# Performance work log

Measured on AMD Instinct MI355X. Metric: run time of the kernel, lower is better.

## Reference

```python
import jax, jax.numpy as jnp
import numpy as np

N = 2_097_152   # number of samples
C = 16          # n_classes
DECAY = 0.8


def setup_inputs() -> dict:
    key = jax.random.key(0)
    k1, k2 = jax.random.split(key)
    logits = jax.random.normal(k1, (N, C), dtype=jnp.float32)
    targets = jax.random.randint(k2, (N,), 0, C)
    weight = jnp.ones((C,), dtype=jnp.float32)  # EMA class-weight buffer
    return {"logits": logits, "targets": targets, "weight": weight}


def reference(logits, targets, weight):
    # Single-pass histogram (replaces the per-class Python loop in the source)
    counts = jax.ops.segment_sum(
        jnp.ones_like(targets, dtype=logits.dtype), targets, num_segments=C
    )  # [C]
    new_w = counts.sum() / counts          # total / per-class count
    new_w = new_w / new_w.sum()            # normalize to sum 1
    w = DECAY * weight + (1.0 - DECAY) * new_w  # EMA-updated weight [C]

    # Weighted cross-entropy, mean reduction (torch semantics:
    # sum(w[y_i] * nll_i) / sum(w[y_i]))
    logp = jax.nn.log_softmax(logits, axis=-1)                       # [N, C]
    nll = -jnp.take_along_axis(logp, targets[:, None], axis=-1)[:, 0]  # [N]
    sw = w[targets]                                                  # [N]
    return jnp.sum(sw * nll) / jnp.sum(sw)
```

## Files before the change

### kernel.cpp

```cpp
#include <hip/hip_runtime.h>

#define NCLS 16
#define DECAY 0.8f

__device__ __forceinline__ float sel16(float4 q0, float4 q1, float4 q2,
                                       float4 q3, int t) {
    float4 sv = (t & 8) ? ((t & 4) ? q3 : q2) : ((t & 4) ? q1 : q0);
    const float lo = (t & 1) ? sv.y : sv.x;
    const float hi = (t & 1) ? sv.w : sv.z;
    return (t & 2) ? hi : lo;
}

__device__ __forceinline__ float esum4(float4 v) {
    return __expf(v.x) + __expf(v.y) + __expf(v.z) + __expf(v.w);
}

__global__ void __launch_bounds__(256, 4)
dwce_fused_kernel(const float4* __restrict__ logits4,
                  const int4*   __restrict__ targets4,
                  float2* __restrict__ partials, int n) {
    __shared__ unsigned int cnt[4][NCLS];
    __shared__ float       snll[4][NCLS];

    const int tid = threadIdx.x;
    const int wid = tid >> 6;
    if (tid < 64) { cnt[tid >> 4][tid & 15] = 0u; snll[tid >> 4][tid & 15] = 0.f; }
    __syncthreads();

    const int gid  = blockIdx.x * blockDim.x + tid;
    const int nth  = gridDim.x * blockDim.x;
    const int ngrp = n >> 2;

    for (int g = gid; g < ngrp; g += nth) {
        const int4 t = targets4[g];
        const float4* base = logits4 + ((size_t)g << 4);
        float4 a0 = base[0],  a1 = base[1],  a2 = base[2],  a3 = base[3];
        float4 b0 = base[4],  b1 = base[5],  b2 = base[6],  b3 = base[7];
        float4 c0 = base[8],  c1 = base[9],  c2 = base[10], c3 = base[11];
        float4 d0 = base[12], d1 = base[13], d2 = base[14], d3 = base[15];

        const float S0 = esum4(a0) + esum4(a1) + esum4(a2) + esum4(a3);
        const float S1 = esum4(b0) + esum4(b1) + esum4(b2) + esum4(b3);
        const float S2 = esum4(c0) + esum4(c1) + esum4(c2) + esum4(c3);
        const float S3 = esum4(d0) + esum4(d1) + esum4(d2) + esum4(d3);

        const float x0 = sel16(a0, a1, a2, a3, t.x);
        const float x1 = sel16(b0, b1, b2, b3, t.y);
        const float x2 = sel16(c0, c1, c2, c3, t.z);
        const float x3 = sel16(d0, d1, d2, d3, t.w);

        atomicAdd(&snll[wid][t.x], __logf(S0) - x0);
        atomicAdd(&snll[wid][t.y], __logf(S1) - x1);
        atomicAdd(&snll[wid][t.z], __logf(S2) - x2);
        atomicAdd(&snll[wid][t.w], __logf(S3) - x3);
        atomicAdd(&cnt[wid][t.x], 1u);
        atomicAdd(&cnt[wid][t.y], 1u);
        atomicAdd(&cnt[wid][t.z], 1u);
        atomicAdd(&cnt[wid][t.w], 1u);
    }
    __syncthreads();

    if (tid < NCLS) {
        const unsigned int c =
            cnt[0][tid] + cnt[1][tid] + cnt[2][tid] + cnt[3][tid];
        const float s =
            snll[0][tid] + snll[1][tid] + snll[2][tid] + snll[3][tid];
        partials[tid * gridDim.x + blockIdx.x] = make_float2((float)c, s);
    }
}

__global__ void __launch_bounds__(1024)
dwce_final_kernel(const float2* __restrict__ partials,
                  const float*  __restrict__ weight,
                  int nb, int n, float* __restrict__ out) {
    const int tid  = threadIdx.x;
    const int c    = tid >> 6;
    const int lane = tid & 63;

    float  cacc = 0.f;
    double sacc = 0.0;
    for (int b = lane; b < nb; b += 64) {
        const float2 p = partials[c * nb + b];
        cacc += p.x;
        sacc += (double)p.y;
    }
    #pragma unroll
    for (int off = 32; off > 0; off >>= 1) {
        cacc += __shfl_xor(cacc, off);
        sacc += __shfl_xor(sacc, off);
    }

    __shared__ float  scnt[NCLS];
    __shared__ double ssum[NCLS];
    if (lane == 0) { scnt[c] = cacc; ssum[c] = sacc; }
    __syncthreads();

    if (tid < NCLS) {
        const float  cn = scnt[tid];
        const double sn = ssum[tid];

        const float raw = (float)n / cn;
        float s = raw;
        s += __shfl_xor(s, 1);
        s += __shfl_xor(s, 2);
        s += __shfl_xor(s, 4);
        s += __shfl_xor(s, 8);
        const float w = DECAY * weight[tid] + (1.0f - DECAY) * (raw / s);

        double A = (double)w * sn;
        double B = (double)w * (double)cn;
        A += __shfl_xor(A, 1); B += __shfl_xor(B, 1);
        A += __shfl_xor(A, 2); B += __shfl_xor(B, 2);
        A += __shfl_xor(A, 4); B += __shfl_xor(B, 4);
        A += __shfl_xor(A, 8); B += __shfl_xor(B, 8);
        if (tid == 0) out[0] = (float)(A / B);
    }
}

extern "C" void kernel_launch(void* const* d_in, const int* in_sizes, int n_in,
                              void* d_out, int out_size, void* d_ws, size_t ws_size,
                              hipStream_t stream) {
    const float* logits  = (const float*)d_in[0];
    const int*   targets = (const int*)d_in[1];
    const float* weight  = (const float*)d_in[2];
    float* out = (float*)d_out;

    float2* partials = (float2*)d_ws;

    const int n = in_sizes[1];

    int nb = 2048;
    const int ws_cap = (int)(ws_size / (NCLS * sizeof(float2)));
    if (nb > ws_cap) nb = ws_cap;
    if (nb < 1) nb = 1;

    dwce_fused_kernel<<<nb, 256, 0, stream>>>((const float4*)logits,
                                              (const int4*)targets,
                                              partials, n);
    dwce_final_kernel<<<1, 1024, 0, stream>>>(partials, weight, nb, n, out);
}
```

Before: 38.65 us.

## Process two rows per thread from split halves with more blocks

Each thread now handles two rows, one from each half of the batch, instead of four consecutive rows. Adjacent threads therefore read adjacent 64-byte rows, which improves coalescing over the earlier 256-byte stride, and per-thread register pressure drops. The launch-bounds occupancy hint goes from 4 to 8 and the grid doubles to 4096 blocks. The trade-offs are scalar target loads instead of int4, a larger partials buffer for the final reduction, and an odd n leaving its last row unprocessed.

```diff
diff --git a/kernel.cpp b/kernel.cpp
--- a/kernel.cpp
+++ b/kernel.cpp
@@ -15,9 +15,9 @@
     return __expf(v.x) + __expf(v.y) + __expf(v.z) + __expf(v.w);
 }
 
-__global__ void __launch_bounds__(256, 4)
+__global__ void __launch_bounds__(256, 8)
 dwce_fused_kernel(const float4* __restrict__ logits4,
-                  const int4*   __restrict__ targets4,
+                  const int*    __restrict__ targets,
                   float2* __restrict__ partials, int n) {
     __shared__ unsigned int cnt[4][NCLS];
     __shared__ float       snll[4][NCLS];
@@ -29,34 +29,25 @@
 
     const int gid  = blockIdx.x * blockDim.x + tid;
     const int nth  = gridDim.x * blockDim.x;
-    const int ngrp = n >> 2;
+    const int half = n >> 1;
 
-    for (int g = gid; g < ngrp; g += nth) {
-        const int4 t = targets4[g];
-        const float4* base = logits4 + ((size_t)g << 4);
-        float4 a0 = base[0],  a1 = base[1],  a2 = base[2],  a3 = base[3];
-        float4 b0 = base[4],  b1 = base[5],  b2 = base[6],  b3 = base[7];
-        float4 c0 = base[8],  c1 = base[9],  c2 = base[10], c3 = base[11];
-        float4 d0 = base[12], d1 = base[13], d2 = base[14], d3 = base[15];
+    for (int i = gid; i < half; i += nth) {
+        const float4* ra = logits4 + (size_t)i * 4;
+        const float4* rb = logits4 + ((size_t)i + half) * 4;
+        float4 a0 = ra[0], a1 = ra[1], a2 = ra[2], a3 = ra[3];
+        float4 b0 = rb[0], b1 = rb[1], b2 = rb[2], b3 = rb[3];
+        const int ta = targets[i];
+        const int tb = targets[i + half];
 
-        const float S0 = esum4(a0) + esum4(a1) + esum4(a2) + esum4(a3);
-        const float S1 = esum4(b0) + esum4(b1) + esum4(b2) + esum4(b3);
-        const float S2 = esum4(c0) + esum4(c1) + esum4(c2) + esum4(c3);
-        const float S3 = esum4(d0) + esum4(d1) + esum4(d2) + esum4(d3);
+        const float Sa = esum4(a0) + esum4(a1) + esum4(a2) + esum4(a3);
+        const float Sb = esum4(b0) + esum4(b1) + esum4(b2) + esum4(b3);
+        const float xa = sel16(a0, a1, a2, a3, ta);
+        const float xb = sel16(b0, b1, b2, b3, tb);
 
-        const float x0 = sel16(a0, a1, a2, a3, t.x);
-        const float x1 = sel16(b0, b1, b2, b3, t.y);
-        const float x2 = sel16(c0, c1, c2, c3, t.z);
-        const float x3 = sel16(d0, d1, d2, d3, t.w);
-
-        atomicAdd(&snll[wid][t.x], __logf(S0) - x0);
-        atomicAdd(&snll[wid][t.y], __logf(S1) - x1);
-        atomicAdd(&snll[wid][t.z], __logf(S2) - x2);
-        atomicAdd(&snll[wid][t.w], __logf(S3) - x3);
-        atomicAdd(&cnt[wid][t.x], 1u);
-        atomicAdd(&cnt[wid][t.y], 1u);
-        atomicAdd(&cnt[wid][t.z], 1u);
-        atomicAdd(&cnt[wid][t.w], 1u);
+        atomicAdd(&snll[wid][ta], __logf(Sa) - xa);
+        atomicAdd(&snll[wid][tb], __logf(Sb) - xb);
+        atomicAdd(&cnt[wid][ta], 1u);
+        atomicAdd(&cnt[wid][tb], 1u);
     }
     __syncthreads();
 
@@ -129,13 +120,12 @@
 
     const int n = in_sizes[1];
 
-    int nb = 2048;
+    int nb = 4096;
     const int ws_cap = (int)(ws_size / (NCLS * sizeof(float2)));
     if (nb > ws_cap) nb = ws_cap;
     if (nb < 1) nb = 1;
 
-    dwce_fused_kernel<<<nb, 256, 0, stream>>>((const float4*)logits,
-                                              (const int4*)targets,
+    dwce_fused_kernel<<<nb, 256, 0, stream>>>((const float4*)logits, targets,
                                               partials, n);
     dwce_final_kernel<<<1, 1024, 0, stream>>>(partials, weight, nb, n, out);
 }
```

Measured after the change: 45.89 us. +18.7%, slower.
